# Optimization experiments

Measured on AMD Instinct MI355X. Metric: run time of the kernel, lower is better.

Reference implementation:

```python
import jax, jax.numpy as jnp
import numpy as np

NUM_HEADS = 8
SIZE_Q = 512
SIZE_K = 512
SIZE_V = 512
B, S = 2, 2048


def setup_inputs() -> dict:
    key = jax.random.key(0)
    ks = jax.random.split(key, 16)
    Hk = SIZE_K  # num_heads * head_size_k
    Hv = SIZE_V  # num_heads * head_size_v
    inp = {
        "k": jax.random.normal(ks[0], (B, S, SIZE_K), jnp.float32),
        "v": jax.random.normal(ks[1], (B, S, SIZE_V), jnp.float32),
        "q": jax.random.normal(ks[2], (B, S, SIZE_Q), jnp.float32),
        "mask": jax.random.randint(ks[3], (S, S), 0, 2).astype(jnp.bool_),
        "spatial_bias": jax.random.normal(ks[4], (1, NUM_HEADS, S, S), jnp.float32),
        # Linear params stored as [in, out]; y = x @ W + b
        "Wq": jax.random.normal(ks[5], (SIZE_Q, Hk), jnp.float32) / np.sqrt(SIZE_Q),
        "bq": jnp.zeros((Hk,), jnp.float32),
        "Wk": jax.random.normal(ks[6], (SIZE_K, Hk), jnp.float32) / np.sqrt(SIZE_K),
        "bk": jnp.zeros((Hk,), jnp.float32),
        "Wv": jax.random.normal(ks[7], (SIZE_V, Hv), jnp.float32) / np.sqrt(SIZE_V),
        "bv": jnp.zeros((Hv,), jnp.float32),
        "Wo": jax.random.normal(ks[8], (Hv, SIZE_V), jnp.float32) / np.sqrt(Hv),
        "bo": jnp.zeros((SIZE_V,), jnp.float32),
    }
    return inp


def reference(k, v, q, mask, spatial_bias, Wq, bq, Wk, bk, Wv, bv, Wo, bo):
    batch, sk = k.shape[0], k.shape[1]
    sq = q.shape[1]
    hdk = Wk.shape[1] // NUM_HEADS
    hdv = Wv.shape[1] // NUM_HEADS
    # QKV projections -> [B, H, S, hd]
    kp = (k @ Wk + bk).reshape(batch, sk, NUM_HEADS, hdk).transpose(0, 2, 1, 3)
    vp = (v @ Wv + bv).reshape(batch, sk, NUM_HEADS, hdv).transpose(0, 2, 1, 3)
    qp = (q @ Wq + bq).reshape(batch, sq, NUM_HEADS, hdk).transpose(0, 2, 1, 3)
    qp = qp / jnp.sqrt(jnp.asarray(hdk, qp.dtype))
    # Scores with additive spatial bias and boolean mask (2D mask -> [1,1,S,S])
    scores = jnp.einsum("bhqd,bhkd->bhqk", qp, kp) + spatial_bias
    scores = jnp.where(mask[None, None, :, :], scores, -jnp.inf)
    attn = jax.nn.softmax(scores, axis=-1)  # dropout=0 (eval)
    ctx = jnp.einsum("bhqk,bhkd->bhqd", attn, vp)
    ctx = ctx.transpose(0, 2, 1, 3).reshape(batch, sq, NUM_HEADS * hdv)
    return ctx @ Wo + bo
```

## Files before the change

kernel.cpp:

```cpp
#include <hip/hip_runtime.h>
#include <hip/hip_bf16.h>

#define S_LEN 2048
#define NH 8
#define HD 64
#define CH 512
#define NEG_BIG (-3.0e38f)
#define KHALF 1024
#define CTXP_STRIDE (2 * NH * S_LEN * HD)
#define ML_STRIDE   (2 * NH * S_LEN)
#define LDS_T (128 * 36)
#define OUTP_STRIDE (4096 * 512)

typedef __bf16 bf16;
typedef bf16 bf16x8 __attribute__((ext_vector_type(8)));
typedef bf16 bf16x4 __attribute__((ext_vector_type(4)));
typedef float floatx4 __attribute__((ext_vector_type(4)));

typedef const unsigned int __attribute__((address_space(1)))* gas1_t;
typedef unsigned int __attribute__((address_space(3)))* las3_t;
__device__ __forceinline__ void gll16(const void* g, void* l) {
    __builtin_amdgcn_global_load_lds((gas1_t)g, (las3_t)l, 16, 0, 0);
}

__global__ void detect_mask_kernel(const unsigned char* __restrict__ mb,
                                   int* __restrict__ flag_out) {
    __shared__ int s1, s3;
    if (threadIdx.x == 0) { s1 = 0; s3 = 0; }
    __syncthreads();
    int any1 = 0, any3 = 0;
    int base = threadIdx.x * 16;
    for (int i = base; i < base + 16; ++i) {
        unsigned char bch = mb[i];
        int m = i & 3;
        if (bch != 0) {
            if (m == 1) any1 = 1;
            if (m == 2 || m == 3) any3 = 1;
        }
    }
    if (any1) atomicOr(&s1, 1);
    if (any3) atomicOr(&s3, 1);
    __syncthreads();
    if (threadIdx.x == 0) {
        int f = 0;
        if (s1) f = 1;
        else if (s3) f = 2;
        *flag_out = f;
    }
}

__global__ __launch_bounds__(256) void prep_weights_kernel(
    const float* __restrict__ Wq, const float* __restrict__ Wk,
    const float* __restrict__ Wv, const float* __restrict__ Wo,
    bf16* __restrict__ WThi, bf16* __restrict__ WTlo)
{
    __shared__ float tile[64][65];
    const int t = threadIdx.x;
    const int n0 = blockIdx.x * 64;
    const int k0 = blockIdx.y * 64;
    const int mat = blockIdx.z;
    const float* W = (mat == 0) ? Wq : (mat == 1) ? Wk : (mat == 2) ? Wv : Wo;
    bf16* hi = WThi + (size_t)mat * (CH * CH);
    bf16* lo = WTlo + (size_t)mat * (CH * CH);
#pragma unroll
    for (int i = 0; i < 4; ++i) {
        int row = (t >> 4) + 16 * i;
        int c4 = (t & 15) << 2;
        float4 f = *(const float4*)(W + (size_t)(k0 + row) * CH + n0 + c4);
        tile[row][c4 + 0] = f.x; tile[row][c4 + 1] = f.y;
        tile[row][c4 + 2] = f.z; tile[row][c4 + 3] = f.w;
    }
    __syncthreads();
#pragma unroll
    for (int i = 0; i < 4; ++i) {
        int nr = (t >> 4) + 16 * i;
        int k4 = (t & 15) << 2;
        bf16x4 h, l;
#pragma unroll
        for (int j = 0; j < 4; ++j) {
            float x = tile[k4 + j][nr];
            bf16 hv = (bf16)x;
            h[j] = hv;
            l[j] = (bf16)(x - (float)hv);
        }
        *(bf16x4*)(hi + (size_t)(n0 + nr) * CH + k0 + k4) = h;
        *(bf16x4*)(lo + (size_t)(n0 + nr) * CH + k0 + k4) = l;
    }
}

__device__ __forceinline__ void gemm_bf16_tile(
    bf16* __restrict__ As_hi, bf16* __restrict__ As_lo,
    bf16* __restrict__ Bs_hi, bf16* __restrict__ Bs_lo,
    const float* __restrict__ IN, const bf16* __restrict__ WThi,
    const bf16* __restrict__ WTlo, const float* __restrict__ BI,
    float* __restrict__ OUT, bf16* __restrict__ OBF,
    const float* __restrict__ ML, float scale, int mode,
    int kbeg, int kiters)
{
    const int t = threadIdx.x;
    const int w = t >> 6;
    const int lane = t & 63;
    const int m16 = lane & 15;
    const int quad = lane >> 4;
    const int m0 = blockIdx.y * 128;
    const int n0 = blockIdx.x * 128;

    const int arow = t >> 1;
    const int akc  = (t & 1) << 4;

    floatx4 acc[2][8];
#pragma unroll
    for (int mi = 0; mi < 2; ++mi)
#pragma unroll
        for (int ni = 0; ni < 8; ++ni) {
            acc[mi][ni][0] = 0.f; acc[mi][ni][1] = 0.f;
            acc[mi][ni][2] = 0.f; acc[mi][ni][3] = 0.f;
        }

    float4 af[4];
    bf16x8 pbh[2], pbl[2];

    auto loadA = [&](int k0) {
        if (ML) {
            int col = k0 + akc;
            int hh = col >> 6, dd = col & 63;
            int row = m0 + arow;
            int bb = row >> 11, ss = row & (S_LEN - 1);
            size_t prow = ((size_t)bb * NH + hh) * S_LEN + ss;
            float m0v = ML[prow * 2],                 l0v = ML[prow * 2 + 1];
            float m1v = ML[(ML_STRIDE + prow) * 2],   l1v = ML[(ML_STRIDE + prow) * 2 + 1];
            float mx = fmaxf(m0v, m1v);
            float e0 = __expf(m0v - mx), e1 = __expf(m1v - mx);
            float den = e0 * l0v + e1 * l1v;
            float inv = den > 0.f ? 1.f / den : 0.f;
            float a0 = e0 * inv, a1 = e1 * inv;
            const float* p0 = IN + prow * HD + dd;
            const float* p1 = p0 + CTXP_STRIDE;
#pragma unroll
            for (int j = 0; j < 4; ++j) {
                float4 c0 = ((const float4*)p0)[j];
                float4 c1 = ((const float4*)p1)[j];
                af[j].x = a0 * c0.x + a1 * c1.x;
                af[j].y = a0 * c0.y + a1 * c1.y;
                af[j].z = a0 * c0.z + a1 * c1.z;
                af[j].w = a0 * c0.w + a1 * c1.w;
            }
        } else {
            const float* p = IN + (size_t)(m0 + arow) * CH + k0 + akc;
            af[0] = ((const float4*)p)[0];
            af[1] = ((const float4*)p)[1];
            af[2] = ((const float4*)p)[2];
            af[3] = ((const float4*)p)[3];
        }
    };
    auto loadB = [&](int k0) {
        const bf16* ph = WThi + (size_t)(n0 + arow) * CH + k0 + akc;
        const bf16* pl = WTlo + (size_t)(n0 + arow) * CH + k0 + akc;
        pbh[0] = ((const bf16x8*)ph)[0]; pbh[1] = ((const bf16x8*)ph)[1];
        pbl[0] = ((const bf16x8*)pl)[0]; pbl[1] = ((const bf16x8*)pl)[1];
    };
    auto stage = [&](int buf) {
        int base = buf * LDS_T;
#pragma unroll
        for (int hh = 0; hh < 2; ++hh) {
            bf16x8 h, l;
#pragma unroll
            for (int j = 0; j < 8; ++j) {
                float x = ((const float*)&af[2 * hh])[j];
                bf16 hv = (bf16)x;
                h[j] = hv;
                l[j] = (bf16)(x - (float)hv);
            }
            *(bf16x8*)&As_hi[base + arow * 36 + akc + 8 * hh] = h;
            *(bf16x8*)&As_lo[base + arow * 36 + akc + 8 * hh] = l;
        }
        *(bf16x8*)&Bs_hi[base + arow * 36 + akc + 0] = pbh[0];
        *(bf16x8*)&Bs_hi[base + arow * 36 + akc + 8] = pbh[1];
        *(bf16x8*)&Bs_lo[base + arow * 36 + akc + 0] = pbl[0];
        *(bf16x8*)&Bs_lo[base + arow * 36 + akc + 8] = pbl[1];
    };

    loadA(kbeg); loadB(kbeg);
    stage(0);
    if (kiters > 1) { loadA(kbeg + 32); loadB(kbeg + 32); }
    __syncthreads();
    int cur = 0;

    for (int ks = 0; ks < kiters; ++ks) {
        int cb = cur * LDS_T;
        bf16x8 bh[8], bl[8];
#pragma unroll
        for (int ni = 0; ni < 8; ++ni) {
            bh[ni] = *(const bf16x8*)&Bs_hi[cb + (16 * ni + m16) * 36 + 8 * quad];
            bl[ni] = *(const bf16x8*)&Bs_lo[cb + (16 * ni + m16) * 36 + 8 * quad];
        }
#pragma unroll
        for (int mi = 0; mi < 2; ++mi) {
            bf16x8 ah = *(const bf16x8*)&As_hi[cb + (32 * w + 16 * mi + m16) * 36 + 8 * quad];
            bf16x8 al = *(const bf16x8*)&As_lo[cb + (32 * w + 16 * mi + m16) * 36 + 8 * quad];
#pragma unroll
            for (int ni = 0; ni < 8; ++ni) {
                acc[mi][ni] = __builtin_amdgcn_mfma_f32_16x16x32_bf16(ah, bh[ni], acc[mi][ni], 0, 0, 0);
                acc[mi][ni] = __builtin_amdgcn_mfma_f32_16x16x32_bf16(ah, bl[ni], acc[mi][ni], 0, 0, 0);
                acc[mi][ni] = __builtin_amdgcn_mfma_f32_16x16x32_bf16(al, bh[ni], acc[mi][ni], 0, 0, 0);
            }
        }
        if (ks + 1 < kiters) {
            stage(cur ^ 1);
            if (ks + 2 < kiters) { loadA(kbeg + 32 * (ks + 2)); loadB(kbeg + 32 * (ks + 2)); }
        }
        __syncthreads();
        cur ^= 1;
    }

#pragma unroll
    for (int mi = 0; mi < 2; ++mi) {
#pragma unroll
        for (int r = 0; r < 4; ++r) {
            int row = m0 + 32 * w + 16 * mi + 4 * quad + r;
            int bb = row >> 11;
            int ss = row & (S_LEN - 1);
#pragma unroll
            for (int ni = 0; ni < 8; ++ni) {
                int col = n0 + 16 * ni + m16;
                float v = BI ? (acc[mi][ni][r] + BI[col]) * scale
                             : acc[mi][ni][r] * scale;
                if (mode == 0) {
                    int hh = col >> 6, dd = col & 63;
                    OUT[(((size_t)bb * NH + hh) * S_LEN + ss) * HD + dd] = v;
                } else if (mode == 3) {
                    int hh = col >> 6, dd = col & 63;
                    OBF[((size_t)(bb * NH + hh) * S_LEN + ss) * HD
                        + (((dd >> 3) ^ (ss & 7)) << 3) + (dd & 7)] = (bf16)v;
                } else if (mode == 4) {
                    int hh = col >> 6, dd = col & 63;
                    OBF[((size_t)(bb * NH + hh) * HD + dd) * S_LEN
                        + (ss & ~63) + ((((ss >> 3) & 7) ^ (dd & 7)) << 3) + (ss & 7)] = (bf16)v;
                } else {
                    OUT[(size_t)row * CH + col] = v;
                }
            }
        }
    }
}

__global__ __launch_bounds__(256, 2) void qkv_gemm_kernel(
    const float* __restrict__ q_in, const float* __restrict__ k_in,
    const float* __restrict__ v_in,
    const bf16* __restrict__ WThi, const bf16* __restrict__ WTlo,
    const float* __restrict__ bq, const float* __restrict__ bk,
    const float* __restrict__ bv,
    float* __restrict__ qp, bf16* __restrict__ kswz, bf16* __restrict__ vswz)
{
    __shared__ __attribute__((aligned(16))) bf16 As_hi[2 * LDS_T];
    __shared__ __attribute__((aligned(16))) bf16 As_lo[2 * LDS_T];
    __shared__ __attribute__((aligned(16))) bf16 Bs_hi[2 * LDS_T];
    __shared__ __attribute__((aligned(16))) bf16 Bs_lo[2 * LDS_T];
    int z = blockIdx.z;
    if (z == 0)
        gemm_bf16_tile(As_hi, As_lo, Bs_hi, Bs_lo, q_in,
                       WThi, WTlo, bq, qp, nullptr, nullptr, 0.125f, 0, 0, 16);
    else if (z == 1)
        gemm_bf16_tile(As_hi, As_lo, Bs_hi, Bs_lo, k_in,
                       WThi + (size_t)CH * CH, WTlo + (size_t)CH * CH, bk,
                       nullptr, kswz, nullptr, 1.0f, 3, 0, 16);
    else
        gemm_bf16_tile(As_hi, As_lo, Bs_hi, Bs_lo, v_in,
                       WThi + (size_t)2 * CH * CH, WTlo + (size_t)2 * CH * CH, bv,
                       nullptr, vswz, nullptr, 1.0f, 4, 0, 16);
}

__global__ __launch_bounds__(256, 2) void out_gemm_kernel(
    const float* __restrict__ ctxp, const float* __restrict__ ml,
    const bf16* __restrict__ WThi, const bf16* __restrict__ WTlo,
    float* __restrict__ outp)
{
    __shared__ __attribute__((aligned(16))) bf16 As_hi[2 * LDS_T];
    __shared__ __attribute__((aligned(16))) bf16 As_lo[2 * LDS_T];
    __shared__ __attribute__((aligned(16))) bf16 Bs_hi[2 * LDS_T];
    __shared__ __attribute__((aligned(16))) bf16 Bs_lo[2 * LDS_T];
    int z = blockIdx.z;
    gemm_bf16_tile(As_hi, As_lo, Bs_hi, Bs_lo, ctxp,
                   WThi + (size_t)3 * CH * CH, WTlo + (size_t)3 * CH * CH,
                   nullptr, outp + (size_t)z * OUTP_STRIDE, nullptr, ml,
                   1.0f, 2, z * 256, 8);
}

__global__ __launch_bounds__(256) void add_out_kernel(
    const float* __restrict__ outp, const float* __restrict__ bo,
    float* __restrict__ out)
{
    int idx = blockIdx.x * 256 + threadIdx.x;
    int col4 = (idx & 127) << 2;
    float4 a = ((const float4*)outp)[idx];
    float4 b = ((const float4*)(outp + OUTP_STRIDE))[idx];
    float4 c = *(const float4*)(bo + col4);
    float4 o;
    o.x = a.x + b.x + c.x;
    o.y = a.y + b.y + c.y;
    o.z = a.z + b.z + c.z;
    o.w = a.w + b.w + c.w;
    ((float4*)out)[idx] = o;
}

__global__ __launch_bounds__(256, 4) void attn_kernel(
    const float* __restrict__ qp, const bf16* __restrict__ kswz,
    const bf16* __restrict__ vswz, const float* __restrict__ bias,
    const void* __restrict__ mask, const int* __restrict__ flagp,
    float* __restrict__ ctxp, float* __restrict__ ml)
{
    __shared__ __attribute__((aligned(16))) bf16 Kt[2][64 * 64];
    __shared__ __attribute__((aligned(16))) bf16 Vt[2][64 * 64];
    __shared__ __attribute__((aligned(16))) bf16 Pbf[64 * 72];

    const int t    = threadIdx.x;
    const int w    = t >> 6;
    const int lane = t & 63;
    const int m16  = lane & 15;
    const int quad = lane >> 4;
    const int mx7  = m16 & 7;

    const int p  = blockIdx.x + 32 * (blockIdx.y + 8 * blockIdx.z);
    const int l  = (p & 7) * 128 + (p >> 3);
    const int b  = l & 1;
    const int kz = (l >> 1) & 1;
    const int h  = (l >> 2) & 7;
    const int qi = l >> 5;

    const int q0   = qi * 64;
    const int bh   = b * NH + h;
    const int flag = *flagp;
    const int kbeg = kz * KHALF;

    bf16x8 qf[2];
    {
        const float* qrow =
            qp + ((size_t)bh * S_LEN + q0 + 16 * w + m16) * HD + 8 * quad;
#pragma unroll
        for (int c = 0; c < 2; ++c) {
            float4 f0 = *(const float4*)(qrow + 32 * c);
            float4 f1 = *(const float4*)(qrow + 32 * c + 4);
            bf16x8 v;
            v[0] = (bf16)f0.x; v[1] = (bf16)f0.y; v[2] = (bf16)f0.z; v[3] = (bf16)f0.w;
            v[4] = (bf16)f1.x; v[5] = (bf16)f1.y; v[6] = (bf16)f1.z; v[7] = (bf16)f1.w;
            qf[c] = v;
        }
    }

    floatx4 ctxa[4];
    float mrow[4], lrow[4];
#pragma unroll
    for (int tt = 0; tt < 4; ++tt) { ctxa[tt][0]=0.f; ctxa[tt][1]=0.f; ctxa[tt][2]=0.f; ctxa[tt][3]=0.f; }
#pragma unroll
    for (int r = 0; r < 4; ++r) { mrow[r] = NEG_BIG; lrow[r] = 0.f; }

    const int qrow0 = q0 + 16 * w + 4 * quad;
    const float* bbase = bias + ((size_t)h * S_LEN + qrow0) * S_LEN + m16;
    const unsigned char* mb8  = (const unsigned char*)mask + (size_t)qrow0 * S_LEN + m16;
    const unsigned int*  mb32 = (const unsigned int*)mask  + (size_t)qrow0 * S_LEN + m16;

    float bnext[16]; unsigned mnext[16]; float mb[16];
    auto prefetchBM = [&](int k0) {
        if (flag == 1) {
#pragma unroll
            for (int r = 0; r < 4; ++r)
#pragma unroll
                for (int tt = 0; tt < 4; ++tt)
                    mnext[4 * r + tt] = mb8[(size_t)r * S_LEN + k0 + 16 * tt];
        } else {
#pragma unroll
            for (int r = 0; r < 4; ++r)
#pragma unroll
                for (int tt = 0; tt < 4; ++tt)
                    mnext[4 * r + tt] = mb32[(size_t)r * S_LEN + k0 + 16 * tt];
        }
#pragma unroll
        for (int r = 0; r < 4; ++r)
#pragma unroll
            for (int tt = 0; tt < 4; ++tt)
                bnext[4 * r + tt] = bbase[(size_t)r * S_LEN + k0 + 16 * tt];
    };

    const bf16* kb = kswz + (size_t)bh * S_LEN * HD;
    const bf16* vb = vswz + (size_t)bh * HD * S_LEN;
    const int lrow8 = lane >> 3;
    const int lcol8 = (lane & 7) * 8;

    auto stageKV = [&](int k0, int buf) {
#pragma unroll
        for (int i = 0; i < 2; ++i) {
            int c = 2 * w + i;
            int row = 8 * c + lrow8;
            gll16(kb + (size_t)(k0 + row) * HD + lcol8, &Kt[buf][c * 512]);
            gll16(vb + (size_t)row * S_LEN + k0 + lcol8, &Vt[buf][c * 512]);
        }
    };

    prefetchBM(kbeg);
    stageKV(kbeg, 0);
    __syncthreads();
    int cur = 0;

    for (int k0 = kbeg; k0 < kbeg + KHALF; k0 += 64) {
        const bool more = (k0 + 64 < kbeg + KHALF);
        if (more) stageKV(k0 + 64, cur ^ 1);

#pragma unroll
        for (int j = 0; j < 16; ++j) mb[j] = mnext[j] ? bnext[j] : NEG_BIG;
        if (more) prefetchBM(k0 + 64);

        const bf16* Kc = Kt[cur];
        const bf16* Vc = Vt[cur];
        floatx4 sc[4];
#pragma unroll
        for (int tt = 0; tt < 4; ++tt) { sc[tt][0]=0.f; sc[tt][1]=0.f; sc[tt][2]=0.f; sc[tt][3]=0.f; }
#pragma unroll
        for (int st = 0; st < 2; ++st)
#pragma unroll
            for (int tt = 0; tt < 4; ++tt) {
                bf16x8 kf = *(const bf16x8*)&Kc[(16 * tt + m16) * 64
                                                + (((quad + 4 * st) ^ mx7) << 3)];
                sc[tt] = __builtin_amdgcn_mfma_f32_16x16x32_bf16(qf[st], kf, sc[tt], 0, 0, 0);
            }

        float alpha[4];
#pragma unroll
        for (int r = 0; r < 4; ++r) {
            int lrowq = 16 * w + 4 * quad + r;
            float s[4];
#pragma unroll
            for (int tt = 0; tt < 4; ++tt)
                s[tt] = sc[tt][r] + mb[4 * r + tt];
            float mx = fmaxf(fmaxf(s[0], s[1]), fmaxf(s[2], s[3]));
            mx = fmaxf(mx, __shfl_xor(mx, 1));
            mx = fmaxf(mx, __shfl_xor(mx, 2));
            mx = fmaxf(mx, __shfl_xor(mx, 4));
            mx = fmaxf(mx, __shfl_xor(mx, 8));
            float mnew = fmaxf(mrow[r], mx);
            float al = __expf(mrow[r] - mnew);
            float ls = 0.f;
#pragma unroll
            for (int tt = 0; tt < 4; ++tt) {
                float px = (s[tt] <= -1e37f) ? 0.f : __expf(s[tt] - mnew);
                ls += px;
                Pbf[lrowq * 72 + 16 * tt + m16] = (bf16)px;
            }
            ls += __shfl_xor(ls, 1);
            ls += __shfl_xor(ls, 2);
            ls += __shfl_xor(ls, 4);
            ls += __shfl_xor(ls, 8);
            lrow[r] = lrow[r] * al + ls;
            mrow[r] = mnew;
            alpha[r] = al;
        }
#pragma unroll
        for (int tt = 0; tt < 4; ++tt)
#pragma unroll
            for (int r = 0; r < 4; ++r) ctxa[tt][r] *= alpha[r];

#pragma unroll
        for (int st = 0; st < 2; ++st) {
            bf16x8 pf = *(const bf16x8*)&Pbf[(16 * w + m16) * 72 + 8 * quad + 32 * st];
#pragma unroll
            for (int tt = 0; tt < 4; ++tt) {
                bf16x8 vf = *(const bf16x8*)&Vc[(16 * tt + m16) * 64
                                                + (((quad + 4 * st) ^ mx7) << 3)];
                ctxa[tt] = __builtin_amdgcn_mfma_f32_16x16x32_bf16(pf, vf, ctxa[tt], 0, 0, 0);
            }
        }

        __syncthreads();
        cur ^= 1;
    }

    float* cp = ctxp + (size_t)kz * CTXP_STRIDE;
#pragma unroll
    for (int r = 0; r < 4; ++r) {
        int grow = q0 + 16 * w + 4 * quad + r;
        size_t prow = (size_t)bh * S_LEN + grow;
#pragma unroll
        for (int tt = 0; tt < 4; ++tt)
            cp[prow * HD + 16 * tt + m16] = ctxa[tt][r];
        if (m16 == 0) {
            ml[((size_t)kz * ML_STRIDE + prow) * 2 + 0] = mrow[r];
            ml[((size_t)kz * ML_STRIDE + prow) * 2 + 1] = lrow[r];
        }
    }
}

extern "C" void kernel_launch(void* const* d_in, const int* in_sizes, int n_in,
                              void* d_out, int out_size, void* d_ws, size_t ws_size,
                              hipStream_t stream) {
    const float* k_in = (const float*)d_in[0];
    const float* v_in = (const float*)d_in[1];
    const float* q_in = (const float*)d_in[2];
    const void*  mask = d_in[3];
    const float* bias = (const float*)d_in[4];
    const float* Wq = (const float*)d_in[5];
    const float* bq = (const float*)d_in[6];
    const float* Wk = (const float*)d_in[7];
    const float* bk = (const float*)d_in[8];
    const float* Wv = (const float*)d_in[9];
    const float* bv = (const float*)d_in[10];
    const float* Wo = (const float*)d_in[11];
    const float* bo = (const float*)d_in[12];
    float* out = (float*)d_out;

    char* base = (char*)d_ws;
    float* qp   = (float*)(base);
    float* ctxp = (float*)(base + (8u  << 20));
    float* mlb  = (float*)(base + (24u << 20));
    bf16*  kswz = (bf16*) (base + (25u << 20));
    bf16*  vswz = (bf16*) (base + (29u << 20));
    bf16*  WThi = (bf16*) (base + (33u << 20));
    bf16*  WTlo = (bf16*) (base + (35u << 20));
    float* outp = (float*)(base + (37u << 20));
    int*   flag = (int*)  (base + (53u << 20));

    detect_mask_kernel<<<1, 256, 0, stream>>>((const unsigned char*)mask, flag);
    prep_weights_kernel<<<dim3(8, 8, 4), 256, 0, stream>>>(
        Wq, Wk, Wv, Wo, WThi, WTlo);
    qkv_gemm_kernel<<<dim3(4, 32, 3), 256, 0, stream>>>(
        q_in, k_in, v_in, WThi, WTlo, bq, bk, bv, qp, kswz, vswz);
    attn_kernel<<<dim3(32, 8, 4), 256, 0, stream>>>(
        qp, kswz, vswz, bias, mask, flag, ctxp, mlb);
    out_gemm_kernel<<<dim3(4, 32, 2), 256, 0, stream>>>(
        ctxp, mlb, WThi, WTlo, outp);
    add_out_kernel<<<2048, 256, 0, stream>>>(outp, bo, out);
}
```

Measured before the change: 442.2 us.

## Halve GEMM M-tile to 64 and single-buffer LDS for higher occupancy

The projection GEMM tiles shrink from 128x128 to 64x128, so each wave computes one 16-row strip and twice as many blocks are launched for the QKV and output GEMMs. The double-buffered LDS staging becomes a single buffer with padded stride 40 and two barriers per k-step, and launch bounds rise to 4 blocks per SM. The aim is better CU fill and occupancy on a small GEMM grid, at the cost of less B-tile reuse per block, more barriers, and less load/compute overlap.

```diff
diff --git a/kernel.cpp b/kernel.cpp
--- a/kernel.cpp
+++ b/kernel.cpp
@@ -9,7 +9,6 @@
 #define KHALF 1024
 #define CTXP_STRIDE (2 * NH * S_LEN * HD)
 #define ML_STRIDE   (2 * NH * S_LEN)
-#define LDS_T (128 * 36)
 #define OUTP_STRIDE (4096 * 512)
 
 typedef __bf16 bf16;
@@ -102,27 +101,27 @@
     const int lane = t & 63;
     const int m16 = lane & 15;
     const int quad = lane >> 4;
-    const int m0 = blockIdx.y * 128;
+    const int m0 = blockIdx.y * 64;
     const int n0 = blockIdx.x * 128;
 
-    const int arow = t >> 1;
-    const int akc  = (t & 1) << 4;
-
-    floatx4 acc[2][8];
-#pragma unroll
-    for (int mi = 0; mi < 2; ++mi)
-#pragma unroll
-        for (int ni = 0; ni < 8; ++ni) {
-            acc[mi][ni][0] = 0.f; acc[mi][ni][1] = 0.f;
-            acc[mi][ni][2] = 0.f; acc[mi][ni][3] = 0.f;
-        }
-
-    float4 af[4];
+    const int arow = t >> 2;
+    const int ac8  = (t & 3) << 3;
+    const int brow = t >> 1;
+    const int bkc  = (t & 1) << 4;
+
+    floatx4 acc[8];
+#pragma unroll
+    for (int ni = 0; ni < 8; ++ni) {
+        acc[ni][0] = 0.f; acc[ni][1] = 0.f;
+        acc[ni][2] = 0.f; acc[ni][3] = 0.f;
+    }
+
+    float4 af[2];
     bf16x8 pbh[2], pbl[2];
 
     auto loadA = [&](int k0) {
         if (ML) {
-            int col = k0 + akc;
+            int col = k0 + ac8;
             int hh = col >> 6, dd = col & 63;
             int row = m0 + arow;
             int bb = row >> 11, ss = row & (S_LEN - 1);
@@ -137,7 +136,7 @@
             const float* p0 = IN + prow * HD + dd;
             const float* p1 = p0 + CTXP_STRIDE;
 #pragma unroll
-            for (int j = 0; j < 4; ++j) {
+            for (int j = 0; j < 2; ++j) {
                 float4 c0 = ((const float4*)p0)[j];
                 float4 c1 = ((const float4*)p1)[j];
                 af[j].x = a0 * c0.x + a1 * c1.x;
@@ -146,105 +145,86 @@
                 af[j].w = a0 * c0.w + a1 * c1.w;
             }
         } else {
-            const float* p = IN + (size_t)(m0 + arow) * CH + k0 + akc;
+            const float* p = IN + (size_t)(m0 + arow) * CH + k0 + ac8;
             af[0] = ((const float4*)p)[0];
             af[1] = ((const float4*)p)[1];
-            af[2] = ((const float4*)p)[2];
-            af[3] = ((const float4*)p)[3];
         }
     };
     auto loadB = [&](int k0) {
-        const bf16* ph = WThi + (size_t)(n0 + arow) * CH + k0 + akc;
-        const bf16* pl = WTlo + (size_t)(n0 + arow) * CH + k0 + akc;
+        const bf16* ph = WThi + (size_t)(n0 + brow) * CH + k0 + bkc;
+        const bf16* pl = WTlo + (size_t)(n0 + brow) * CH + k0 + bkc;
         pbh[0] = ((const bf16x8*)ph)[0]; pbh[1] = ((const bf16x8*)ph)[1];
         pbl[0] = ((const bf16x8*)pl)[0]; pbl[1] = ((const bf16x8*)pl)[1];
     };
-    auto stage = [&](int buf) {
-        int base = buf * LDS_T;
-#pragma unroll
-        for (int hh = 0; hh < 2; ++hh) {
-            bf16x8 h, l;
-#pragma unroll
-            for (int j = 0; j < 8; ++j) {
-                float x = ((const float*)&af[2 * hh])[j];
-                bf16 hv = (bf16)x;
-                h[j] = hv;
-                l[j] = (bf16)(x - (float)hv);
+    auto stage = [&]() {
+        bf16x8 h, l;
+#pragma unroll
+        for (int j = 0; j < 8; ++j) {
+            float x = ((const float*)&af[0])[j];
+            bf16 hv = (bf16)x;
+            h[j] = hv;
+            l[j] = (bf16)(x - (float)hv);
+        }
+        *(bf16x8*)&As_hi[arow * 40 + ac8] = h;
+        *(bf16x8*)&As_lo[arow * 40 + ac8] = l;
+        *(bf16x8*)&Bs_hi[brow * 40 + bkc + 0] = pbh[0];
+        *(bf16x8*)&Bs_hi[brow * 40 + bkc + 8] = pbh[1];
+        *(bf16x8*)&Bs_lo[brow * 40 + bkc + 0] = pbl[0];
+        *(bf16x8*)&Bs_lo[brow * 40 + bkc + 8] = pbl[1];
+    };
+
+    loadA(kbeg); loadB(kbeg);
+    for (int ks = 0; ks < kiters; ++ks) {
+        __syncthreads();
+        stage();
+        __syncthreads();
+        if (ks + 1 < kiters) { loadA(kbeg + 32 * (ks + 1)); loadB(kbeg + 32 * (ks + 1)); }
+
+        bf16x8 bh[8], bl[8];
+#pragma unroll
+        for (int ni = 0; ni < 8; ++ni) {
+            bh[ni] = *(const bf16x8*)&Bs_hi[(16 * ni + m16) * 40 + 8 * quad];
+            bl[ni] = *(const bf16x8*)&Bs_lo[(16 * ni + m16) * 40 + 8 * quad];
+        }
+        bf16x8 ah = *(const bf16x8*)&As_hi[(16 * w + m16) * 40 + 8 * quad];
+        bf16x8 al = *(const bf16x8*)&As_lo[(16 * w + m16) * 40 + 8 * quad];
+#pragma unroll
+        for (int ni = 0; ni < 8; ++ni) {
+            acc[ni] = __builtin_amdgcn_mfma_f32_16x16x32_bf16(ah, bh[ni], acc[ni], 0, 0, 0);
+            acc[ni] = __builtin_amdgcn_mfma_f32_16x16x32_bf16(ah, bl[ni], acc[ni], 0, 0, 0);
+            acc[ni] = __builtin_amdgcn_mfma_f32_16x16x32_bf16(al, bh[ni], acc[ni], 0, 0, 0);
+        }
+    }
+
+#pragma unroll
+    for (int r = 0; r < 4; ++r) {
+        int row = m0 + 16 * w + 4 * quad + r;
+        int bb = row >> 11;
+        int ss = row & (S_LEN - 1);
+#pragma unroll
+        for (int ni = 0; ni < 8; ++ni) {
+            int col = n0 + 16 * ni + m16;
+            float v = BI ? (acc[ni][r] + BI[col]) * scale
+                         : acc[ni][r] * scale;
+            if (mode == 0) {
+                int hh = col >> 6, dd = col & 63;
+                OUT[(((size_t)bb * NH + hh) * S_LEN + ss) * HD + dd] = v;
+            } else if (mode == 3) {
+                int hh = col >> 6, dd = col & 63;
+                OBF[((size_t)(bb * NH + hh) * S_LEN + ss) * HD
+                    + (((dd >> 3) ^ (ss & 7)) << 3) + (dd & 7)] = (bf16)v;
+            } else if (mode == 4) {
+                int hh = col >> 6, dd = col & 63;
+                OBF[((size_t)(bb * NH + hh) * HD + dd) * S_LEN
+                    + (ss & ~63) + ((((ss >> 3) & 7) ^ (dd & 7)) << 3) + (ss & 7)] = (bf16)v;
+            } else {
+                OUT[(size_t)row * CH + col] = v;
             }
-            *(bf16x8*)&As_hi[base + arow * 36 + akc + 8 * hh] = h;
-            *(bf16x8*)&As_lo[base + arow * 36 + akc + 8 * hh] = l;
-        }
-        *(bf16x8*)&Bs_hi[base + arow * 36 + akc + 0] = pbh[0];
-        *(bf16x8*)&Bs_hi[base + arow * 36 + akc + 8] = pbh[1];
-        *(bf16x8*)&Bs_lo[base + arow * 36 + akc + 0] = pbl[0];
-        *(bf16x8*)&Bs_lo[base + arow * 36 + akc + 8] = pbl[1];
-    };
-
-    loadA(kbeg); loadB(kbeg);
-    stage(0);
-    if (kiters > 1) { loadA(kbeg + 32); loadB(kbeg + 32); }
-    __syncthreads();
-    int cur = 0;
-
-    for (int ks = 0; ks < kiters; ++ks) {
-        int cb = cur * LDS_T;
-        bf16x8 bh[8], bl[8];
-#pragma unroll
-        for (int ni = 0; ni < 8; ++ni) {
-            bh[ni] = *(const bf16x8*)&Bs_hi[cb + (16 * ni + m16) * 36 + 8 * quad];
-            bl[ni] = *(const bf16x8*)&Bs_lo[cb + (16 * ni + m16) * 36 + 8 * quad];
-        }
-#pragma unroll
-        for (int mi = 0; mi < 2; ++mi) {
-            bf16x8 ah = *(const bf16x8*)&As_hi[cb + (32 * w + 16 * mi + m16) * 36 + 8 * quad];
-            bf16x8 al = *(const bf16x8*)&As_lo[cb + (32 * w + 16 * mi + m16) * 36 + 8 * quad];
-#pragma unroll
-            for (int ni = 0; ni < 8; ++ni) {
-                acc[mi][ni] = __builtin_amdgcn_mfma_f32_16x16x32_bf16(ah, bh[ni], acc[mi][ni], 0, 0, 0);
-                acc[mi][ni] = __builtin_amdgcn_mfma_f32_16x16x32_bf16(ah, bl[ni], acc[mi][ni], 0, 0, 0);
-                acc[mi][ni] = __builtin_amdgcn_mfma_f32_16x16x32_bf16(al, bh[ni], acc[mi][ni], 0, 0, 0);
-            }
-        }
-        if (ks + 1 < kiters) {
-            stage(cur ^ 1);
-            if (ks + 2 < kiters) { loadA(kbeg + 32 * (ks + 2)); loadB(kbeg + 32 * (ks + 2)); }
-        }
-        __syncthreads();
-        cur ^= 1;
-    }
-
-#pragma unroll
-    for (int mi = 0; mi < 2; ++mi) {
-#pragma unroll
-        for (int r = 0; r < 4; ++r) {
-            int row = m0 + 32 * w + 16 * mi + 4 * quad + r;
-            int bb = row >> 11;
-            int ss = row & (S_LEN - 1);
-#pragma unroll
-            for (int ni = 0; ni < 8; ++ni) {
-                int col = n0 + 16 * ni + m16;
-                float v = BI ? (acc[mi][ni][r] + BI[col]) * scale
-                             : acc[mi][ni][r] * scale;
-                if (mode == 0) {
-                    int hh = col >> 6, dd = col & 63;
-                    OUT[(((size_t)bb * NH + hh) * S_LEN + ss) * HD + dd] = v;
-                } else if (mode == 3) {
-                    int hh = col >> 6, dd = col & 63;
-                    OBF[((size_t)(bb * NH + hh) * S_LEN + ss) * HD
-                        + (((dd >> 3) ^ (ss & 7)) << 3) + (dd & 7)] = (bf16)v;
-                } else if (mode == 4) {
-                    int hh = col >> 6, dd = col & 63;
-                    OBF[((size_t)(bb * NH + hh) * HD + dd) * S_LEN
-                        + (ss & ~63) + ((((ss >> 3) & 7) ^ (dd & 7)) << 3) + (ss & 7)] = (bf16)v;
-                } else {
-                    OUT[(size_t)row * CH + col] = v;
-                }
-            }
-        }
-    }
-}
-
-__global__ __launch_bounds__(256, 2) void qkv_gemm_kernel(
+        }
+    }
+}
+
+__global__ __launch_bounds__(256, 4) void qkv_gemm_kernel(
     const float* __restrict__ q_in, const float* __restrict__ k_in,
     const float* __restrict__ v_in,
     const bf16* __restrict__ WThi, const bf16* __restrict__ WTlo,
@@ -252,10 +232,10 @@
     const float* __restrict__ bv,
     float* __restrict__ qp, bf16* __restrict__ kswz, bf16* __restrict__ vswz)
 {
-    __shared__ __attribute__((aligned(16))) bf16 As_hi[2 * LDS_T];
-    __shared__ __attribute__((aligned(16))) bf16 As_lo[2 * LDS_T];
-    __shared__ __attribute__((aligned(16))) bf16 Bs_hi[2 * LDS_T];
-    __shared__ __attribute__((aligned(16))) bf16 Bs_lo[2 * LDS_T];
+    __shared__ __attribute__((aligned(16))) bf16 As_hi[64 * 40];
+    __shared__ __attribute__((aligned(16))) bf16 As_lo[64 * 40];
+    __shared__ __attribute__((aligned(16))) bf16 Bs_hi[128 * 40];
+    __shared__ __attribute__((aligned(16))) bf16 Bs_lo[128 * 40];
     int z = blockIdx.z;
     if (z == 0)
         gemm_bf16_tile(As_hi, As_lo, Bs_hi, Bs_lo, q_in,
@@ -270,15 +250,15 @@
                        nullptr, vswz, nullptr, 1.0f, 4, 0, 16);
 }
 
-__global__ __launch_bounds__(256, 2) void out_gemm_kernel(
+__global__ __launch_bounds__(256, 4) void out_gemm_kernel(
     const float* __restrict__ ctxp, const float* __restrict__ ml,
     const bf16* __restrict__ WThi, const bf16* __restrict__ WTlo,
     float* __restrict__ outp)
 {
-    __shared__ __attribute__((aligned(16))) bf16 As_hi[2 * LDS_T];
-    __shared__ __attribute__((aligned(16))) bf16 As_lo[2 * LDS_T];
-    __shared__ __attribute__((aligned(16))) bf16 Bs_hi[2 * LDS_T];
-    __shared__ __attribute__((aligned(16))) bf16 Bs_lo[2 * LDS_T];
+    __shared__ __attribute__((aligned(16))) bf16 As_hi[64 * 40];
+    __shared__ __attribute__((aligned(16))) bf16 As_lo[64 * 40];
+    __shared__ __attribute__((aligned(16))) bf16 Bs_hi[128 * 40];
+    __shared__ __attribute__((aligned(16))) bf16 Bs_lo[128 * 40];
     int z = blockIdx.z;
     gemm_bf16_tile(As_hi, As_lo, Bs_hi, Bs_lo, ctxp,
                    WThi + (size_t)3 * CH * CH, WTlo + (size_t)3 * CH * CH,
@@ -520,11 +500,11 @@
     detect_mask_kernel<<<1, 256, 0, stream>>>((const unsigned char*)mask, flag);
     prep_weights_kernel<<<dim3(8, 8, 4), 256, 0, stream>>>(
         Wq, Wk, Wv, Wo, WThi, WTlo);
-    qkv_gemm_kernel<<<dim3(4, 32, 3), 256, 0, stream>>>(
+    qkv_gemm_kernel<<<dim3(4, 64, 3), 256, 0, stream>>>(
         q_in, k_in, v_in, WThi, WTlo, bq, bk, bv, qp, kswz, vswz);
     attn_kernel<<<dim3(32, 8, 4), 256, 0, stream>>>(
         qp, kswz, vswz, bias, mask, flag, ctxp, mlb);
-    out_gemm_kernel<<<dim3(4, 32, 2), 256, 0, stream>>>(
+    out_gemm_kernel<<<dim3(4, 64, 2), 256, 0, stream>>>(
         ctxp, mlb, WThi, WTlo, outp);
     add_out_kernel<<<2048, 256, 0, stream>>>(outp, bo, out);
 }
```

Result: faster. 357.8 us (-19.1%).
